# Performance work log

Measured on AMD Instinct MI355X. Metric: run time of the kernel, lower is better.

The kernel has to match this reference:

```python
import jax, jax.numpy as jnp
import numpy as np

DIM = 512
NUM_HEADS = 8
HEAD_DIM = DIM // NUM_HEADS
SR = 2
LN_EPS = 1e-5


def setup_inputs() -> dict:
    key = jax.random.key(0)
    ks = jax.random.split(key, 12)
    B, H, W = 8, 32, 32
    N = H * W
    s = 0.02
    return {
        "x": jax.random.normal(ks[0], (B, N, DIM), jnp.float32),
        "H": H,
        "W": W,
        # weights stored as [in, out] (torch Linear applies x @ W.T + b)
        "q_w": jax.random.normal(ks[1], (DIM, DIM), jnp.float32) * s,
        "q_b": jnp.zeros((DIM,), jnp.float32),
        "kv_w": jax.random.normal(ks[2], (DIM, 2 * DIM), jnp.float32) * s,
        "kv_b": jnp.zeros((2 * DIM,), jnp.float32),
        "sr_w": jax.random.normal(ks[3], (DIM, DIM, SR, SR), jnp.float32) * s,  # OIHW
        "sr_b": jnp.zeros((DIM,), jnp.float32),
        "ln_g": jnp.ones((DIM,), jnp.float32),
        "ln_b": jnp.zeros((DIM,), jnp.float32),
        "proj_w": jax.random.normal(ks[4], (DIM, DIM), jnp.float32) * s,
        "proj_b": jnp.zeros((DIM,), jnp.float32),
    }


def reference(x, H, W, q_w, q_b, kv_w, kv_b, sr_w, sr_b, ln_g, ln_b, proj_w, proj_b):
    B, N, C = x.shape
    hd = HEAD_DIM
    scale = hd ** -0.5

    # q: [B, nh, N, hd]
    q = (x @ q_w + q_b).reshape(B, N, NUM_HEADS, hd).transpose(0, 2, 1, 3)

    # spatial reduction conv (stride=kernel=SR) + LayerNorm
    x2d = x.transpose(0, 2, 1).reshape(B, C, H, W)
    x2d = jax.lax.conv_general_dilated(
        x2d, sr_w, window_strides=(SR, SR), padding="VALID",
        dimension_numbers=("NCHW", "OIHW", "NCHW")) + sr_b[None, :, None, None]
    Nk = x2d.shape[2] * x2d.shape[3]
    x_kv = x2d.reshape(B, C, Nk).transpose(0, 2, 1)  # [B, Nk, C]
    mu = x_kv.mean(-1, keepdims=True)
    var = ((x_kv - mu) ** 2).mean(-1, keepdims=True)
    x_kv = (x_kv - mu) * jax.lax.rsqrt(var + LN_EPS) * ln_g + ln_b

    kv = x_kv @ kv_w + kv_b  # [B, Nk, 2C]
    k, v = kv[..., :C], kv[..., C:]
    # Faithful to torch: reshape folds C/hd into kv-sequence axis -> M = Nk*num_heads,
    # shared (broadcast) across all query heads.
    M = Nk * NUM_HEADS
    k = k.reshape(B, M, hd)
    v = v.reshape(B, M, hd)

    attn = jnp.einsum("bhnd,bmd->bhnm", q, k) * scale  # [B, nh, N, M]
    attn = jax.nn.softmax(attn, axis=-1)
    out = jnp.einsum("bhnm,bmd->bhnd", attn, v)  # [B, nh, N, hd]
    out = out.transpose(0, 2, 1, 3).reshape(B, N, C)
    return out @ proj_w + proj_b
```

## Files before the change

### kernel.cpp

```cpp
#include <hip/hip_runtime.h>
#include <hip/hip_bf16.h>
#include <stdint.h>

typedef __attribute__((ext_vector_type(8))) short short8;
typedef __attribute__((ext_vector_type(4))) float f32x4;

#define MFMA(A, B, C) __builtin_amdgcn_mfma_f32_16x16x32_bf16(A, B, C, 0, 0, 0)

__device__ inline uint32_t bfrne(float f) {
  uint32_t u = __float_as_uint(f);
  return (u + 0x7FFFu + ((u >> 16) & 1u)) >> 16;
}

__device__ inline uint32_t pkrne(float a, float b) {
  union { __hip_bfloat162 v; uint32_t u; } c;
  c.v.x = __float2bfloat16(a);
  c.v.y = __float2bfloat16(b);
  return c.u;
}

__device__ inline float fexp2(float x) { return __builtin_amdgcn_exp2f(x); }

__device__ inline void gload16(const short* g, short* l) {
  __builtin_amdgcn_global_load_lds(
      (const __attribute__((address_space(1))) void*)g,
      (__attribute__((address_space(3))) void*)l, 16, 0, 0);
}

__global__ __launch_bounds__(256) void prep_all_kernel(
    const float* __restrict__ sr_w, const float* __restrict__ kv_w,
    const float* __restrict__ q_w, const float* __restrict__ proj_w,
    const float* __restrict__ x,
    short* __restrict__ WcThi, short* __restrict__ kvThi,
    short* __restrict__ qThi, short* __restrict__ pThi,
    short* __restrict__ xhi) {
  __shared__ float tile[32][33];
  const int blk = blockIdx.x;
  if (blk < 4096) {
    int t = blk * 256 + threadIdx.x;
    int kk = t & 2047, o = t >> 11;
    float v = sr_w[(size_t)o * 2048 + ((kk & 511) << 2) + (kk >> 9)];
    WcThi[t] = (short)bfrne(v);
    return;
  }
  if (blk >= 5120) {
    int t = (blk - 5120) * 256 + threadIdx.x;
    float4 v0 = *(const float4*)&x[(size_t)t * 8];
    float4 v1 = *(const float4*)&x[(size_t)t * 8 + 4];
    uint4 pk;
    pk.x = pkrne(v0.x, v0.y);
    pk.y = pkrne(v0.z, v0.w);
    pk.z = pkrne(v1.x, v1.y);
    pk.w = pkrne(v1.z, v1.w);
    *(uint4*)&xhi[(size_t)t * 8] = pk;
    return;
  }
  const float* in; short* ohi; int N, bx, by;
  if (blk < 4608) {
    in = kv_w; ohi = kvThi; N = 1024;
    int i = blk - 4096; bx = i & 31; by = i >> 5;
  } else if (blk < 4864) {
    in = q_w; ohi = qThi; N = 512;
    int i = blk - 4608; bx = i & 15; by = i >> 4;
  } else {
    in = proj_w; ohi = pThi; N = 512;
    int i = blk - 4864; bx = i & 15; by = i >> 4;
  }
  const int K = 512;
  const int tx = threadIdx.x & 31, ty = threadIdx.x >> 5;
#pragma unroll
  for (int i = 0; i < 4; ++i)
    tile[ty + i * 8][tx] = in[(size_t)(by * 32 + ty + i * 8) * N + bx * 32 + tx];
  __syncthreads();
#pragma unroll
  for (int i = 0; i < 4; ++i) {
    int n = bx * 32 + ty + i * 8;
    float v = tile[tx][ty + i * 8];
    ohi[(size_t)n * K + by * 32 + tx] = (short)bfrne(v);
  }
}

__global__ __launch_bounds__(256) void ln_kernel(
    const float* __restrict__ X, const float* __restrict__ g,
    const float* __restrict__ bta, short* __restrict__ hi) {
  const int row = blockIdx.x, t = threadIdx.x;
  size_t idx = (size_t)row * 512 + t * 2;
  const size_t PS = (size_t)2048 * 512;
  float2 a0 = *(const float2*)&X[idx];
  float2 a1 = *(const float2*)&X[idx + PS];
  float2 a2 = *(const float2*)&X[idx + 2 * PS];
  float2 a3 = *(const float2*)&X[idx + 3 * PS];
  float x0 = a0.x + a1.x + a2.x + a3.x;
  float x1 = a0.y + a1.y + a2.y + a3.y;
  float s = x0 + x1, sq = x0 * x0 + x1 * x1;
#pragma unroll
  for (int off = 1; off < 64; off <<= 1) {
    s += __shfl_xor(s, off);
    sq += __shfl_xor(sq, off);
  }
  __shared__ float rs[4], rq[4];
  int wid = t >> 6;
  if ((t & 63) == 0) { rs[wid] = s; rq[wid] = sq; }
  __syncthreads();
  s = rs[0] + rs[1] + rs[2] + rs[3];
  sq = rq[0] + rq[1] + rq[2] + rq[3];
  float mu = s * (1.f / 512), var = sq * (1.f / 512) - mu * mu;
  float inv = rsqrtf(var + 1e-5f);
  float2 gg = *(const float2*)&g[t * 2], bb = *(const float2*)&bta[t * 2];
  float o0 = (x0 - mu) * inv * gg.x + bb.x;
  float o1 = (x1 - mu) * inv * gg.y + bb.y;
  *(uint32_t*)&hi[idx] = pkrne(o0, o1);
}

__global__ void kv_post_kernel(const float* __restrict__ KV1, const float* __restrict__ KV2,
                               short* __restrict__ Kf, short* __restrict__ Vf) {
  const int blk = blockIdx.x;
  if (blk < 4096) {
    int t = blk * 256 + threadIdx.x;
    int j = t & 7, l = (t >> 3) & 63, i = (t >> 9) & 7, tt = (t >> 12) & 31, b = t >> 17;
    int qi = l & 15, g = l >> 4, h2 = i & 1, mf = i >> 1;
    int m = tt * 64 + mf * 16 + qi, d = h2 * 32 + g * 8 + j;
    size_t idx = ((size_t)b * 256 + (m >> 3)) * 1024 + (m & 7) * 64 + d;
    Kf[t] = (short)bfrne(KV1[idx] + KV2[idx]);
  } else {
    int t = (blk - 4096) * 256 + threadIdx.x;
    int j = t & 7, l = (t >> 3) & 63, i = (t >> 9) & 7, tt = (t >> 12) & 31, b = t >> 17;
    int qi = l & 15, g = l >> 4, df = i & 3, ks2 = i >> 2;
    int mm = tt * 64 + ks2 * 32 + g * 8 + j, dd = df * 16 + qi;
    size_t idx = ((size_t)b * 256 + (mm >> 3)) * 1024 + 512 + (mm & 7) * 64 + dd;
    Vf[t] = (short)bfrne(KV1[idx] + KV2[idx]);
  }
}

template <bool GATHER, int OMODE>
__device__ __forceinline__ void gemm_body(
    short* ldsraw,
    const short* __restrict__ Ahi, const short* __restrict__ BThi,
    const float* __restrict__ bias, float* __restrict__ C,
    short* __restrict__ Chi, float oscale,
    int M, int N, int lda, int ldb, int klen,
    int bxx, int byy, int bzz) {
  typedef short (*ldsA_t)[64][8];
  typedef short (*ldsB_t)[128][8];
  ldsA_t ldsA = (ldsA_t)ldsraw;
  ldsB_t ldsB = (ldsB_t)(ldsraw + 4 * 64 * 8);
  const int tid = threadIdx.x, lane = tid & 63, wave = tid >> 6;
  const int g = lane >> 4, qi = lane & 15;
  const int row0 = bxx * 64, col0 = byy * 128;
  const int kz = bzz * klen;
  float* Cz = C + (size_t)bzz * M * N;
  const bool dobias = (bzz == 0);
  f32x4 acc[4][2] = {};
  const int arow = tid & 63, akg = tid >> 6;
  const int bsm = tid & 127, bk2 = (tid >> 7) * 2;

  for (int k0 = kz; k0 < kz + klen; k0 += 32) {
    __syncthreads();
    size_t ao;
    if (GATHER) {
      int row = row0 + arow;
      int bi = row >> 8, p = row & 255;
      int col = k0 + akg * 8;
      int seg = col >> 9, cc = col & 511;
      int n = (2 * (p >> 4) + (seg >> 1)) * 32 + 2 * (p & 15) + (seg & 1);
      ao = ((size_t)bi * 1024 + n) * 512 + cc;
    } else {
      ao = (size_t)(row0 + arow) * lda + k0 + akg * 8;
    }
    gload16(&Ahi[ao], &ldsA[akg][arow][0]);
#pragma unroll
    for (int c = 0; c < 2; ++c) {
      size_t bo = (size_t)(col0 + bsm) * ldb + k0 + (bk2 + c) * 8;
      gload16(&BThi[bo], &ldsB[bk2 + c][bsm][0]);
    }
    __syncthreads();
    short8 ah[4], bh[2];
#pragma unroll
    for (int i = 0; i < 4; ++i)
      ah[i] = *(const short8*)&ldsA[g][i * 16 + qi][0];
#pragma unroll
    for (int j = 0; j < 2; ++j)
      bh[j] = *(const short8*)&ldsB[g][wave * 32 + j * 16 + qi][0];
#pragma unroll
    for (int i = 0; i < 4; ++i)
#pragma unroll
      for (int j = 0; j < 2; ++j)
        acc[i][j] = MFMA(ah[i], bh[j], acc[i][j]);
  }
#pragma unroll
  for (int i = 0; i < 4; ++i)
#pragma unroll
    for (int j = 0; j < 2; ++j) {
      int colb = col0 + wave * 32 + j * 16 + qi;
      float bs = dobias ? bias[colb] : 0.f;
#pragma unroll
      for (int r = 0; r < 4; ++r) {
        int row = row0 + i * 16 + g * 4 + r;
        if (OMODE == 0) {
          Cz[(size_t)row * N + colb] = acc[i][j][r] + bs;
        } else {
          Chi[(size_t)row * N + colb] = (short)bfrne((acc[i][j][r] + bs) * oscale);
        }
      }
    }
}

template <bool GATHER, int OMODE>
__global__ __launch_bounds__(256) void gemm_1p(
    const short* __restrict__ Ahi, const short* __restrict__ BThi,
    const float* __restrict__ bias, float* __restrict__ C,
    short* __restrict__ Chi, float oscale,
    int M, int N, int lda, int ldb, int klen) {
  __shared__ short lds[6144];
  gemm_body<GATHER, OMODE>(lds, Ahi, BThi, bias, C, Chi, oscale,
                           M, N, lda, ldb, klen,
                           blockIdx.x, blockIdx.y, blockIdx.z);
}

__global__ __launch_bounds__(256) void conv_q_kernel(
    const short* __restrict__ xhi, const short* __restrict__ WcThi,
    const float* __restrict__ sr_b, float* __restrict__ Cbuf,
    const short* __restrict__ qThi, const float* __restrict__ q_b,
    short* __restrict__ Qhi, float qscale) {
  __shared__ short lds[6144];
  const int blk = blockIdx.x;
  if (blk < 512) {
    int bx = blk & 31, by = (blk >> 5) & 3, bz = blk >> 7;
    gemm_body<true, 0>(lds, xhi, WcThi, sr_b, Cbuf, nullptr, 1.f,
                       2048, 512, 512, 2048, 512, bx, by, bz);
  } else {
    int i = blk - 512;
    int bx = i & 127, by = i >> 7;
    gemm_body<false, 1>(lds, xhi, qThi, q_b, nullptr, Qhi, qscale,
                        8192, 512, 512, 512, 512, bx, by, 0);
  }
}

__device__ __forceinline__ void ld8(short8 (&dst)[8], const short* base) {
#pragma unroll
  for (int i = 0; i < 8; ++i)
    dst[i] = *(const short8*)&base[(size_t)i * 512];
}

__device__ __forceinline__ void attn_tile(
    const short8 (&kr)[8], const short8 (&vr)[8], const short8 (&qh)[2][2],
    f32x4 (&lacc)[2], f32x4 (&oacc)[2][4], short* Psw, int g, int qi, int swz) {
  const short8 ones = {(short)0x3F80, (short)0x3F80, (short)0x3F80, (short)0x3F80,
                       (short)0x3F80, (short)0x3F80, (short)0x3F80, (short)0x3F80};
  f32x4 s[2][4] = {};
  __builtin_amdgcn_s_setprio(1);
#pragma unroll
  for (int mf = 0; mf < 4; ++mf)
#pragma unroll
    for (int qc = 0; qc < 2; ++qc) {
      s[qc][mf] = MFMA(kr[mf * 2 + 0], qh[qc][0], s[qc][mf]);
      s[qc][mf] = MFMA(kr[mf * 2 + 1], qh[qc][1], s[qc][mf]);
    }
  __builtin_amdgcn_s_setprio(0);
#pragma unroll
  for (int qc = 0; qc < 2; ++qc)
#pragma unroll
    for (int mf = 0; mf < 4; ++mf) {
      uint32_t u0 = __float_as_uint(fexp2(s[qc][mf][0]));
      uint32_t u1 = __float_as_uint(fexp2(s[qc][mf][1]));
      uint32_t u2 = __float_as_uint(fexp2(s[qc][mf][2]));
      uint32_t u3 = __float_as_uint(fexp2(s[qc][mf][3]));
      uint2 hp;
      hp.x = (u0 >> 16) | (u1 & 0xffff0000u);
      hp.y = (u2 >> 16) | (u3 & 0xffff0000u);
      int uw = ((mf * 4 + g) ^ swz) << 2;
      *(uint2*)&Psw[qc * 1024 + qi * 64 + uw] = hp;
    }
#pragma unroll
  for (int qc = 0; qc < 2; ++qc)
#pragma unroll
    for (int ks2 = 0; ks2 < 2; ++ks2) {
      int ur = ((ks2 * 8 + g * 2) ^ swz) << 2;
      short8 pa = *(const short8*)&Psw[qc * 1024 + qi * 64 + ur];
      __builtin_amdgcn_s_setprio(1);
      lacc[qc] = MFMA(ones, pa, lacc[qc]);
#pragma unroll
      for (int df = 0; df < 4; ++df)
        oacc[qc][df] = MFMA(vr[ks2 * 4 + df], pa, oacc[qc][df]);
      __builtin_amdgcn_s_setprio(0);
    }
}

__global__ __launch_bounds__(256, 2) void attn_kernel(
    const short* __restrict__ Qhi, const short* __restrict__ Kf,
    const short* __restrict__ Vf, short* __restrict__ Ohi) {
  __shared__ short Ps[4][2][1024];
  const int tid = threadIdx.x, lane = tid & 63, wave = tid >> 6;
  const int g = lane >> 4, qi = lane & 15;
  const int h = blockIdx.y, b = blockIdx.z;
  const int n0 = blockIdx.x * 128 + wave * 32;
  const int swz = (qi & 7) << 1;
  short* Psw = &Ps[wave][0][0];

  short8 qh[2][2];
#pragma unroll
  for (int qc = 0; qc < 2; ++qc) {
    const size_t qrow = ((size_t)b * 1024 + n0 + qc * 16 + qi) * 512 + h * 64;
#pragma unroll
    for (int ks = 0; ks < 2; ++ks)
      qh[qc][ks] = *(const short8*)&Qhi[qrow + (ks * 4 + g) * 8];
  }
  f32x4 lacc[2] = {};
  f32x4 oacc[2][4] = {};
  const short* Kb = Kf + (size_t)b * 131072 + lane * 8;
  const short* Vb = Vf + (size_t)b * 131072 + lane * 8;

  short8 kA[8], kB[8], vr[8];
  ld8(kA, Kb);
  for (int it = 0; it < 16; ++it) {
    const short* tK = Kb + (size_t)it * 8192;
    const short* tV = Vb + (size_t)it * 8192;
    ld8(kB, tK + 4096);
    ld8(vr, tV);
    attn_tile(kA, vr, qh, lacc, oacc, Psw, g, qi, swz);
    if (it < 15) ld8(kA, tK + 8192);
    ld8(vr, tV + 4096);
    attn_tile(kB, vr, qh, lacc, oacc, Psw, g, qi, swz);
  }
#pragma unroll
  for (int qc = 0; qc < 2; ++qc) {
    float linv = 1.f / lacc[qc][0];
    size_t obase = ((size_t)b * 1024 + n0 + qc * 16 + qi) * 512 + h * 64;
#pragma unroll
    for (int df = 0; df < 4; ++df) {
      float o0 = oacc[qc][df][0] * linv, o1 = oacc[qc][df][1] * linv;
      float o2 = oacc[qc][df][2] * linv, o3 = oacc[qc][df][3] * linv;
      uint2 hp;
      hp.x = pkrne(o0, o1);
      hp.y = pkrne(o2, o3);
      *(uint2*)&Ohi[obase + df * 16 + g * 4] = hp;
    }
  }
}

extern "C" void kernel_launch(void* const* d_in, const int* in_sizes, int n_in,
                              void* d_out, int out_size, void* d_ws, size_t ws_size,
                              hipStream_t stream) {
  const float* x      = (const float*)d_in[0];
  const float* q_w    = (const float*)d_in[3];
  const float* q_b    = (const float*)d_in[4];
  const float* kv_w   = (const float*)d_in[5];
  const float* kv_b   = (const float*)d_in[6];
  const float* sr_w   = (const float*)d_in[7];
  const float* sr_b   = (const float*)d_in[8];
  const float* ln_g   = (const float*)d_in[9];
  const float* ln_b   = (const float*)d_in[10];
  const float* proj_w = (const float*)d_in[11];
  const float* proj_b = (const float*)d_in[12];

  char* W = (char*)d_ws;
  const size_t MB = 1024 * 1024;
  short* xhi   = (short*)(W);
  short* WcThi = (short*)(W + 16 * MB);
  float* Cbuf  = (float*)(W + 20 * MB);
  short* LNhi  = (short*)(W + 36 * MB);
  short* kvThi = (short*)(W + 40 * MB);
  short* qThi  = (short*)(W + 42 * MB);
  short* pThi  = (short*)(W + 43 * MB);
  short* Qhi   = (short*)(W + 44 * MB);
  float* KVp   = (float*)(W + 20 * MB);
  short* Kf    = (short*)(W + 36 * MB);
  short* Vf    = (short*)(W + 16 * MB);
  short* Ohi   = (short*)(W);

  prep_all_kernel<<<7168, 256, 0, stream>>>(
      sr_w, kv_w, q_w, proj_w, x, WcThi, kvThi, qThi, pThi, xhi);
  conv_q_kernel<<<1024, 256, 0, stream>>>(
      xhi, WcThi, sr_b, Cbuf, qThi, q_b, Qhi, 0.125f * 1.44269504f);
  ln_kernel<<<2048, 256, 0, stream>>>(Cbuf, ln_g, ln_b, LNhi);
  gemm_1p<false, 0><<<dim3(32, 8, 2), 256, 0, stream>>>(
      LNhi, kvThi, kv_b, KVp, nullptr, 1.f, 2048, 1024, 512, 512, 256);
  kv_post_kernel<<<8192, 256, 0, stream>>>(KVp, KVp + (size_t)2 * MB, Kf, Vf);
  attn_kernel<<<dim3(8, 8, 8), 256, 0, stream>>>(Qhi, Kf, Vf, Ohi);
  gemm_1p<false, 0><<<dim3(128, 4, 1), 256, 0, stream>>>(
      Ohi, pThi, proj_b, (float*)d_out, nullptr, 1.f, 8192, 512, 512, 512, 512);
}
```

Baseline: 130.0 us.

## Software-pipeline QK^T of next tile with softmax pack and PV of current

Splits the attention tile into separate QK, pack (exp and bf16 store to LDS) and PV stages, then reorders the loop so the QK MFMAs for the next key tile are issued between packing and PV of the current tile. K loads run one more tile ahead. The aim is to overlap the exp and LDS work with matrix-core work inside a wave. This raises register pressure (two score buffers plus two K buffers) under the 2-blocks launch bound, which could cause spills.

```diff
diff --git a/kernel.cpp b/kernel.cpp
--- a/kernel.cpp
+++ b/kernel.cpp
@@ -242,21 +242,22 @@
     dst[i] = *(const short8*)&base[(size_t)i * 512];
 }
 
-__device__ __forceinline__ void attn_tile(
-    const short8 (&kr)[8], const short8 (&vr)[8], const short8 (&qh)[2][2],
-    f32x4 (&lacc)[2], f32x4 (&oacc)[2][4], short* Psw, int g, int qi, int swz) {
-  const short8 ones = {(short)0x3F80, (short)0x3F80, (short)0x3F80, (short)0x3F80,
-                       (short)0x3F80, (short)0x3F80, (short)0x3F80, (short)0x3F80};
-  f32x4 s[2][4] = {};
+__device__ __forceinline__ void qk_tile(f32x4 (&s)[2][4], const short8 (&kr)[8],
+                                        const short8 (&qh)[2][2]) {
+  const f32x4 z = {0.f, 0.f, 0.f, 0.f};
   __builtin_amdgcn_s_setprio(1);
 #pragma unroll
   for (int mf = 0; mf < 4; ++mf)
 #pragma unroll
     for (int qc = 0; qc < 2; ++qc) {
-      s[qc][mf] = MFMA(kr[mf * 2 + 0], qh[qc][0], s[qc][mf]);
+      s[qc][mf] = MFMA(kr[mf * 2 + 0], qh[qc][0], z);
       s[qc][mf] = MFMA(kr[mf * 2 + 1], qh[qc][1], s[qc][mf]);
     }
   __builtin_amdgcn_s_setprio(0);
+}
+
+__device__ __forceinline__ void pack_tile(const f32x4 (&s)[2][4], short* Psw,
+                                          int g, int qi, int swz) {
 #pragma unroll
   for (int qc = 0; qc < 2; ++qc)
 #pragma unroll
@@ -271,6 +272,13 @@
       int uw = ((mf * 4 + g) ^ swz) << 2;
       *(uint2*)&Psw[qc * 1024 + qi * 64 + uw] = hp;
     }
+}
+
+__device__ __forceinline__ void pv_tile(const short8 (&vr)[8], short* Psw,
+                                        f32x4 (&lacc)[2], f32x4 (&oacc)[2][4],
+                                        int g, int qi, int swz) {
+  const short8 ones = {(short)0x3F80, (short)0x3F80, (short)0x3F80, (short)0x3F80,
+                       (short)0x3F80, (short)0x3F80, (short)0x3F80, (short)0x3F80};
 #pragma unroll
   for (int qc = 0; qc < 2; ++qc)
 #pragma unroll
@@ -311,16 +319,23 @@
   const short* Vb = Vf + (size_t)b * 131072 + lane * 8;
 
   short8 kA[8], kB[8], vr[8];
+  f32x4 sA[2][4], sB[2][4];
   ld8(kA, Kb);
-  for (int it = 0; it < 16; ++it) {
-    const short* tK = Kb + (size_t)it * 8192;
-    const short* tV = Vb + (size_t)it * 8192;
-    ld8(kB, tK + 4096);
+  ld8(kB, Kb + 4096);
+  qk_tile(sA, kA, qh);
+  for (int t = 0; t < 32; t += 2) {
+    const short* tK = Kb + (size_t)t * 4096;
+    const short* tV = Vb + (size_t)t * 4096;
     ld8(vr, tV);
-    attn_tile(kA, vr, qh, lacc, oacc, Psw, g, qi, swz);
-    if (it < 15) ld8(kA, tK + 8192);
+    if (t < 30) ld8(kA, tK + 8192);
+    pack_tile(sA, Psw, g, qi, swz);
+    qk_tile(sB, kB, qh);
+    pv_tile(vr, Psw, lacc, oacc, g, qi, swz);
     ld8(vr, tV + 4096);
-    attn_tile(kB, vr, qh, lacc, oacc, Psw, g, qi, swz);
+    if (t < 30) ld8(kB, tK + 12288);
+    pack_tile(sB, Psw, g, qi, swz);
+    if (t < 30) qk_tile(sA, kA, qh);
+    pv_tile(vr, Psw, lacc, oacc, g, qi, swz);
   }
 #pragma unroll
   for (int qc = 0; qc < 2; ++qc) {
```

Measured after the change: 128.2 us. No clear change (-1.4%).
